# Kernel tuning notes

Hardware: AMD Instinct MI355X
Metric: run time of the kernel (lower is better)

The kernel has to match this reference:

```python
import jax, jax.numpy as jnp
import numpy as np

NUM_EMBEDDINGS = 50000
EMBEDDING_DIM = 256
NUM_CODEBOOK = 32
NUM_CODEWORD = 64


def setup_inputs() -> dict:
    key = jax.random.key(0)
    k1, k2, k3 = jax.random.split(key, 3)
    tokens = jax.random.randint(k1, (64, 512), 0, NUM_EMBEDDINGS, dtype=jnp.int64 if jax.config.jax_enable_x64 else jnp.int32)
    code = jax.random.normal(k2, (NUM_EMBEDDINGS, NUM_CODEBOOK, NUM_CODEWORD), dtype=jnp.float32)
    codebook = jax.random.normal(k3, (NUM_CODEBOOK, NUM_CODEWORD, EMBEDDING_DIM), dtype=jnp.float32)
    return {"tokens": tokens, "code": code, "codebook": codebook}


def reference(tokens, code, codebook):
    # tokens: (N, W) int; code: (V, B, C); codebook: (B, C, D)
    N, W = tokens.shape
    idx = tokens.reshape(-1)                      # (N*W,)
    gathered = code[idx]                          # (N*W, B, C)
    # NOTE: original softmaxes over dim=-2 = the codebook axis
    weights = jax.nn.softmax(gathered, axis=-2)   # (N*W, B, C)
    # per-codebook weighted sum of codewords, then sum over codebooks
    out = jnp.einsum('mbc,bcd->md', weights, codebook)  # (N*W, D)
    return out.reshape(N, W, EMBEDDING_DIM)
```

## Files before the change

kernel.cpp:

```cpp
#include <hip/hip_runtime.h>
#include <hip/hip_bf16.h>

#define MT 32768
#define KD 2048
#define DD 256
#define NB 32
#define NC 64
#define MTILE 64
#define KC 512
#define NCH 4
#define LOG2E 1.44269504f

typedef short s8v __attribute__((ext_vector_type(8)));
typedef float f4v __attribute__((ext_vector_type(4)));
typedef unsigned short u16;

__device__ __forceinline__ u16 f2bf(float x) {
  unsigned int u = __float_as_uint(x);
  u += 0x7FFFu + ((u >> 16) & 1u);
  return (u16)(u >> 16);
}

__global__ void pack_b(const float* __restrict__ cb, u16* __restrict__ Bp) {
  int idx = blockIdx.x * 256 + threadIdx.x;
  int lane = idx & 63;
  int s = (idx >> 6) & 63;
  int nt = idx >> 12;
  int n = nt * 16 + (lane & 15);
  int kb = s * 32 + (lane >> 4) * 8;
  s8v v;
#pragma unroll
  for (int j = 0; j < 8; ++j) v[j] = (short)f2bf(cb[(size_t)(kb + j) * DD + n]);
  *(s8v*)(Bp + (size_t)idx * 8) = v;
}

__global__ __launch_bounds__(512, 4) void fused_emb(
    const int* __restrict__ tokens, const float* __restrict__ code,
    const u16* __restrict__ Bp, float* __restrict__ out) {
  __shared__ __align__(16) u16 A[MTILE * KC];

  const int t = threadIdx.x;
  const int w = t >> 6, lane = t & 63;
  const int tokb = blockIdx.x * MTILE;
  const int c = lane;
  const int lid = lane & 15, quad = lane >> 4;
  const int mg = w >> 2, ng = w & 3;

  int tok[8];
#pragma unroll
  for (int i = 0; i < 8; ++i) tok[i] = tokens[tokb + w * 8 + i];

  float mx[8], inv[8];
#pragma unroll
  for (int i = 0; i < 8; ++i) {
    const float* row = code + (size_t)tok[i] * KD + c;
    float g[NB];
#pragma unroll
    for (int b = 0; b < NB; ++b) g[b] = row[b * NC];
    float m0 = g[0];
#pragma unroll
    for (int b = 1; b < NB; ++b) m0 = fmaxf(m0, g[b]);
    float s = 0.f;
#pragma unroll
    for (int b = 0; b < NB; ++b) s += exp2f((g[b] - m0) * LOG2E);
    mx[i] = m0;
    inv[i] = 1.0f / s;
  }

  f4v acc[2][4] = {};

  for (int ch = 0; ch < NCH; ++ch) {
#pragma unroll
    for (int i = 0; i < 8; ++i) {
      const int m = w * 8 + i;
      const float* row = code + (size_t)tok[i] * KD + c;
      u16* arow = A + m * KC;
#pragma unroll
      for (int bl = 0; bl < 8; ++bl) {
        const int b = ch * 8 + bl;
        float wv = exp2f((row[b * NC] - mx[i]) * LOG2E) * inv[i];
        const int kl = bl * 64 + c;
        const int grp = (kl >> 3) ^ i;
        arow[(grp << 3) + (kl & 7)] = f2bf(wv);
      }
    }
    __syncthreads();

    auto ldA = [&](int mt, int sl) -> s8v {
      const int m = mg * 32 + mt * 16 + lid;
      const int kl = sl * 32 + quad * 8;
      const int grp = (kl >> 3) ^ (m & 7);
      return *(const s8v*)(A + m * KC + (grp << 3));
    };
    auto ldB = [&](int nt, int sl) -> s8v {
      const int fi = ((ng * 4 + nt) * 64 + ch * 16 + sl) * 64 + lane;
      return *(const s8v*)(Bp + (size_t)fi * 8);
    };

    s8v a0 = ldA(0, 0), a1 = ldA(1, 0);
    s8v bc[4];
#pragma unroll
    for (int nt = 0; nt < 4; ++nt) bc[nt] = ldB(nt, 0);

#pragma unroll 1
    for (int sl = 0; sl < 15; ++sl) {
      s8v a0n = ldA(0, sl + 1), a1n = ldA(1, sl + 1);
      s8v bn[4];
#pragma unroll
      for (int nt = 0; nt < 4; ++nt) bn[nt] = ldB(nt, sl + 1);
#pragma unroll
      for (int nt = 0; nt < 4; ++nt) {
        acc[0][nt] = __builtin_amdgcn_mfma_f32_16x16x32_bf16(a0, bc[nt], acc[0][nt], 0, 0, 0);
        acc[1][nt] = __builtin_amdgcn_mfma_f32_16x16x32_bf16(a1, bc[nt], acc[1][nt], 0, 0, 0);
      }
      a0 = a0n; a1 = a1n;
#pragma unroll
      for (int nt = 0; nt < 4; ++nt) bc[nt] = bn[nt];
    }
#pragma unroll
    for (int nt = 0; nt < 4; ++nt) {
      acc[0][nt] = __builtin_amdgcn_mfma_f32_16x16x32_bf16(a0, bc[nt], acc[0][nt], 0, 0, 0);
      acc[1][nt] = __builtin_amdgcn_mfma_f32_16x16x32_bf16(a1, bc[nt], acc[1][nt], 0, 0, 0);
    }
    __syncthreads();
  }

  float* ob = out + (size_t)(tokb + mg * 32) * DD + ng * 64 + lid;
#pragma unroll
  for (int mt = 0; mt < 2; ++mt)
#pragma unroll
    for (int r = 0; r < 4; ++r) {
      float* p = ob + (size_t)(mt * 16 + quad * 4 + r) * DD;
#pragma unroll
      for (int nt = 0; nt < 4; ++nt) p[nt * 16] = acc[mt][nt][r];
    }
}

extern "C" void kernel_launch(void* const* d_in, const int* in_sizes, int n_in,
                              void* d_out, int out_size, void* d_ws, size_t ws_size,
                              hipStream_t stream) {
  const int* tokens = (const int*)d_in[0];
  const float* code = (const float*)d_in[1];
  const float* codebook = (const float*)d_in[2];
  float* out = (float*)d_out;
  u16* Bp = (u16*)d_ws;

  pack_b<<<256, 256, 0, stream>>>(codebook, Bp);
  fused_emb<<<MT / MTILE, 512, 0, stream>>>(tokens, code, Bp, out);
}
```

Baseline: 564.1 us.

## Split fused softmax-GEMM into softmax-to-bf16 buffer kernel plus LDS-DMA GEMM

Breaks the fused kernel into a build_w kernel, which computes the codebook-axis softmax once per token and writes the bf16 weights to a workspace already in MFMA fragment order. A separate gemm_w kernel then streams those fragments into LDS with global_load_lds and runs the MFMA loop with 32-row tiles. The fused kernel read each gathered code row twice (once for max and sum, once for the weights) and kept exp work on the critical path beside the MFMAs. The split adds a write and a re-read of a 32768x2048 bf16 intermediate (about 128 MB of traffic), plus one more kernel launch.

```diff
diff --git a/kernel.cpp b/kernel.cpp
--- a/kernel.cpp
+++ b/kernel.cpp
@@ -6,17 +6,15 @@
 #define DD 256
 #define NB 32
 #define NC 64
-#define MTILE 64
-#define KC 512
-#define NCH 4
 #define LOG2E 1.44269504f
 
 typedef short s8v __attribute__((ext_vector_type(8)));
 typedef float f4v __attribute__((ext_vector_type(4)));
 typedef unsigned short u16;
+typedef unsigned int u32;
 
 __device__ __forceinline__ u16 f2bf(float x) {
-  unsigned int u = __float_as_uint(x);
+  u32 u = __float_as_uint(x);
   u += 0x7FFFu + ((u >> 16) & 1u);
   return (u16)(u >> 16);
 }
@@ -34,98 +32,96 @@
   *(s8v*)(Bp + (size_t)idx * 8) = v;
 }
 
-__global__ __launch_bounds__(512, 4) void fused_emb(
+__global__ __launch_bounds__(256, 4) void build_w(
     const int* __restrict__ tokens, const float* __restrict__ code,
-    const u16* __restrict__ Bp, float* __restrict__ out) {
-  __shared__ __align__(16) u16 A[MTILE * KC];
+    u16* __restrict__ Wf) {
+  const int t = threadIdx.x;
+  const int w = t >> 6, lane = t & 63;
+  const int mtile = blockIdx.x;
+  const int q = (lane >> 3) & 3, j = lane & 7, shi = lane >> 5;
+
+#pragma unroll 1
+  for (int i = 0; i < 4; ++i) {
+    const int m_local = w * 4 + i;
+    const int m = mtile * 16 + m_local;
+    const int tok = tokens[m];
+    const float* row = code + (size_t)tok * KD + lane;
+    float g[NB];
+#pragma unroll
+    for (int b = 0; b < NB; ++b) g[b] = row[b * NC];
+    float mx = g[0];
+#pragma unroll
+    for (int b = 1; b < NB; ++b) mx = fmaxf(mx, g[b]);
+    float s = 0.f;
+#pragma unroll
+    for (int b = 0; b < NB; ++b) {
+      g[b] = exp2f((g[b] - mx) * LOG2E);
+      s += g[b];
+    }
+    const float inv = 1.0f / s;
+    u16* base = Wf + ((((size_t)mtile * 64 + shi) * 64) + q * 16 + m_local) * 8 + j;
+#pragma unroll
+    for (int b = 0; b < NB; ++b) base[b * 1024] = f2bf(g[b] * inv);
+  }
+}
+
+#define CSTEP 16
+__global__ __launch_bounds__(256, 4) void gemm_w(
+    const u16* __restrict__ Wf, const u16* __restrict__ Bp, float* __restrict__ out) {
+  __shared__ __align__(16) u16 A[2 * CSTEP * 64 * 8];
 
   const int t = threadIdx.x;
   const int w = t >> 6, lane = t & 63;
-  const int tokb = blockIdx.x * MTILE;
-  const int c = lane;
+  const int mb = blockIdx.x;
   const int lid = lane & 15, quad = lane >> 4;
-  const int mg = w >> 2, ng = w & 3;
+  const int ng = w;
 
-  int tok[8];
-#pragma unroll
-  for (int i = 0; i < 8; ++i) tok[i] = tokens[tokb + w * 8 + i];
+  const u16* wfb = Wf + (size_t)mb * 2 * 64 * 64 * 8;
 
-  float mx[8], inv[8];
-#pragma unroll
-  for (int i = 0; i < 8; ++i) {
-    const float* row = code + (size_t)tok[i] * KD + c;
-    float g[NB];
-#pragma unroll
-    for (int b = 0; b < NB; ++b) g[b] = row[b * NC];
-    float m0 = g[0];
-#pragma unroll
-    for (int b = 1; b < NB; ++b) m0 = fmaxf(m0, g[b]);
-    float s = 0.f;
-#pragma unroll
-    for (int b = 0; b < NB; ++b) s += exp2f((g[b] - m0) * LOG2E);
-    mx[i] = m0;
-    inv[i] = 1.0f / s;
-  }
+  auto ldB = [&](int nt, int s) -> s8v {
+    const int fi = ((ng * 4 + nt) * 64 + s) * 64 + lane;
+    return *(const s8v*)(Bp + (size_t)fi * 8);
+  };
 
   f4v acc[2][4] = {};
+  s8v bc[4], bn[4];
+#pragma unroll
+  for (int nt = 0; nt < 4; ++nt) bc[nt] = ldB(nt, 0);
 
-  for (int ch = 0; ch < NCH; ++ch) {
+  for (int ch = 0; ch < 4; ++ch) {
 #pragma unroll
-    for (int i = 0; i < 8; ++i) {
-      const int m = w * 8 + i;
-      const float* row = code + (size_t)tok[i] * KD + c;
-      u16* arow = A + m * KC;
-#pragma unroll
-      for (int bl = 0; bl < 8; ++bl) {
-        const int b = ch * 8 + bl;
-        float wv = exp2f((row[b * NC] - mx[i]) * LOG2E) * inv[i];
-        const int kl = bl * 64 + c;
-        const int grp = (kl >> 3) ^ i;
-        arow[(grp << 3) + (kl & 7)] = f2bf(wv);
-      }
+    for (int r = 0; r < 8; ++r) {
+      const int flat = r * 256 + t;
+      const int mt = flat >> 10;
+      const int rem = flat & 1023;
+      const u16* gp = wfb + ((size_t)mt * 64 * 64 + (size_t)ch * CSTEP * 64 + rem) * 8;
+      u16* lp = A + (size_t)flat * 8;
+      __builtin_amdgcn_global_load_lds(
+          (const __attribute__((address_space(1))) u32*)gp,
+          (__attribute__((address_space(3))) u32*)lp, 16, 0, 0);
     }
     __syncthreads();
 
-    auto ldA = [&](int mt, int sl) -> s8v {
-      const int m = mg * 32 + mt * 16 + lid;
-      const int kl = sl * 32 + quad * 8;
-      const int grp = (kl >> 3) ^ (m & 7);
-      return *(const s8v*)(A + m * KC + (grp << 3));
-    };
-    auto ldB = [&](int nt, int sl) -> s8v {
-      const int fi = ((ng * 4 + nt) * 64 + ch * 16 + sl) * 64 + lane;
-      return *(const s8v*)(Bp + (size_t)fi * 8);
-    };
-
-    s8v a0 = ldA(0, 0), a1 = ldA(1, 0);
-    s8v bc[4];
+#pragma unroll 1
+    for (int sl = 0; sl < CSTEP; ++sl) {
+      const int s = ch * CSTEP + sl;
+      const int sn = (s + 1 < 64) ? s + 1 : 63;
 #pragma unroll
-    for (int nt = 0; nt < 4; ++nt) bc[nt] = ldB(nt, 0);
-
-#pragma unroll 1
-    for (int sl = 0; sl < 15; ++sl) {
-      s8v a0n = ldA(0, sl + 1), a1n = ldA(1, sl + 1);
-      s8v bn[4];
-#pragma unroll
-      for (int nt = 0; nt < 4; ++nt) bn[nt] = ldB(nt, sl + 1);
+      for (int nt = 0; nt < 4; ++nt) bn[nt] = ldB(nt, sn);
+      s8v a0 = *(const s8v*)(A + ((0 * CSTEP + sl) * 64 + lane) * 8);
+      s8v a1 = *(const s8v*)(A + ((1 * CSTEP + sl) * 64 + lane) * 8);
 #pragma unroll
       for (int nt = 0; nt < 4; ++nt) {
         acc[0][nt] = __builtin_amdgcn_mfma_f32_16x16x32_bf16(a0, bc[nt], acc[0][nt], 0, 0, 0);
         acc[1][nt] = __builtin_amdgcn_mfma_f32_16x16x32_bf16(a1, bc[nt], acc[1][nt], 0, 0, 0);
       }
-      a0 = a0n; a1 = a1n;
 #pragma unroll
       for (int nt = 0; nt < 4; ++nt) bc[nt] = bn[nt];
-    }
-#pragma unroll
-    for (int nt = 0; nt < 4; ++nt) {
-      acc[0][nt] = __builtin_amdgcn_mfma_f32_16x16x32_bf16(a0, bc[nt], acc[0][nt], 0, 0, 0);
-      acc[1][nt] = __builtin_amdgcn_mfma_f32_16x16x32_bf16(a1, bc[nt], acc[1][nt], 0, 0, 0);
     }
     __syncthreads();
   }
 
-  float* ob = out + (size_t)(tokb + mg * 32) * DD + ng * 64 + lid;
+  float* ob = out + (size_t)(mb * 32) * DD + ng * 64 + lid;
 #pragma unroll
   for (int mt = 0; mt < 2; ++mt)
 #pragma unroll
@@ -143,8 +139,11 @@
   const float* code = (const float*)d_in[1];
   const float* codebook = (const float*)d_in[2];
   float* out = (float*)d_out;
+
   u16* Bp = (u16*)d_ws;
+  u16* Wf = (u16*)d_ws + (1u << 19);
 
   pack_b<<<256, 256, 0, stream>>>(codebook, Bp);
-  fused_emb<<<MT / MTILE, 512, 0, stream>>>(tokens, code, Bp, out);
+  build_w<<<MT / 16, 256, 0, stream>>>(tokens, code, Wf);
+  gemm_w<<<MT / 32, 256, 0, stream>>>(Wf, Bp, out);
 }
```

New measurement: 676.2 us. 1.2x slower.
